# Optimization experiments

Hardware: AMD Instinct MI355X
Metric: run time of the kernel (lower is better)

## Reference

```python
import jax, jax.numpy as jnp
import numpy as np

HEADS = 8
HEAD_DIM = 80
TEXT_LEN = 77


def setup_inputs() -> dict:
    key = jax.random.key(0)
    ks = jax.random.split(key, 10)
    B, S, QD, CD, ID = 16, 4096, 640, 768, 640
    NV = 10
    s = 0.02
    return {
        "x": jax.random.normal(ks[0], (B, S, QD), jnp.float32),
        "enc": jax.random.normal(ks[1], (B, TEXT_LEN + NV, CD), jnp.float32),
        "Wq": jax.random.normal(ks[2], (QD, ID), jnp.float32) * s,
        "Wvq": jax.random.normal(ks[3], (QD, ID), jnp.float32) * s,
        "Wk": jax.random.normal(ks[4], (CD, ID), jnp.float32) * s,
        "Wv": jax.random.normal(ks[5], (CD, ID), jnp.float32) * s,
        "Wvk": jax.random.normal(ks[6], (CD, ID), jnp.float32) * s,
        "Wvv": jax.random.normal(ks[7], (CD, ID), jnp.float32) * s,
        "Wo": jax.random.normal(ks[8], (ID, QD), jnp.float32) * s,
        "bo": jnp.zeros((QD,), jnp.float32),
    }


def reference(x, enc, Wq, Wvq, Wk, Wv, Wvk, Wvv, Wo, bo):
    # x: [B, S, query_dim]; enc: [B, 77 + Nv, cross_dim]
    B, S, _ = x.shape
    H, D = HEADS, HEAD_DIM
    scale = 1.0 / jnp.sqrt(jnp.asarray(D, x.dtype))

    text_feats = enc[:, :TEXT_LEN]      # [B, 77, CD]
    visual_feats = enc[:, TEXT_LEN:]    # [B, Nv, CD]

    tq = (x @ Wq).reshape(B, S, H, D)
    vq = (x @ Wvq).reshape(B, S, H, D)
    tk = (text_feats @ Wk).reshape(B, TEXT_LEN, H, D)
    tv = (text_feats @ Wv).reshape(B, TEXT_LEN, H, D)
    vk = (visual_feats @ Wvk).reshape(B, -1, H, D)
    vv = (visual_feats @ Wvv).reshape(B, -1, H, D)

    # separate score blocks, then concat along key dim
    text_scores = scale * jnp.einsum("bqhd,bkhd->bhqk", tq, tk)
    visual_scores = scale * jnp.einsum("bqhd,bkhd->bhqk", vq, vk)
    scores = jnp.concatenate([text_scores, visual_scores], axis=-1)  # [B,H,S,Kt+Kv]
    probs = jax.nn.softmax(scores, axis=-1)

    value = jnp.concatenate([tv, vv], axis=1)  # [B, Kt+Kv, H, D]
    out = jnp.einsum("bhqk,bkhd->bqhd", probs, value).reshape(B, S, H * D)
    return out @ Wo + bo
```

## Files before the change

### kernel.cpp

```cpp
#include <hip/hip_runtime.h>

typedef __attribute__((ext_vector_type(8))) short short8;
typedef __attribute__((ext_vector_type(4))) float f32x4;
typedef __attribute__((ext_vector_type(4))) int int4v;

typedef const __attribute__((address_space(1))) void* gas_t;
typedef __attribute__((address_space(3))) void* las_t;

__device__ __forceinline__ unsigned short f2bf(float f) {
  unsigned int u = __float_as_uint(f);
  u += 0x7fffu + ((u >> 16) & 1u);
  return (unsigned short)(u >> 16);
}

__global__ void cvt_bf16_kernel(const float* __restrict__ in,
                                unsigned short* __restrict__ out, int n) {
  int i = (blockIdx.x * 256 + threadIdx.x) * 4;
  if (i + 3 < n) {
    float4 v = *(const float4*)(in + i);
    ushort4 r;
    r.x = f2bf(v.x); r.y = f2bf(v.y); r.z = f2bf(v.z); r.w = f2bf(v.w);
    *(ushort4*)(out + i) = r;
  }
}

__global__ void transpose_cvt_kernel(const float* __restrict__ W,
                                     unsigned short* __restrict__ Wt,
                                     int K, int N) {
  __shared__ float t[32][33];
  int tx = threadIdx.x & 31, ty = threadIdx.x >> 5;
  int k0 = blockIdx.x * 32, n0 = blockIdx.y * 32;
  #pragma unroll
  for (int i = 0; i < 32; i += 8)
    t[ty + i][tx] = W[(size_t)(k0 + ty + i) * N + n0 + tx];
  __syncthreads();
  #pragma unroll
  for (int i = 0; i < 32; i += 8)
    Wt[(size_t)(n0 + ty + i) * K + k0 + tx] = f2bf(t[tx][ty + i]);
}

__global__ void vtrans_kernel(const unsigned short* __restrict__ KV,
                              unsigned short* __restrict__ VtG) {
  int idx = blockIdx.x * 256 + threadIdx.x;
  if (idx >= 16 * 8 * 80 * 96) return;
  int k = idx % 96;
  int d = (idx / 96) % 80;
  int h = (idx / (96 * 80)) % 8;
  int b = idx / (96 * 80 * 8);
  unsigned short v = 0;
  if (k < 87) {
    int base = (k < 77) ? 640 : 1920;
    v = KV[(size_t)(b * 87 + k) * 2560 + base + h * 80 + d];
  }
  VtG[idx] = v;
}

template<bool F32OUT>
__global__ __launch_bounds__(256, 2) void gemm_bt_kernel(
    const unsigned short* __restrict__ A,
    const unsigned short* __restrict__ Bt,
    void* __restrict__ Cptr, const float* __restrict__ bias,
    int M, int N, int K, int NT) {
  __shared__ __align__(16) unsigned short smem[2 * 128 * 64];
  unsigned short* As = smem;
  unsigned short* Bs = smem + 128 * 64;

  const int tid  = threadIdx.x;
  const int wave = tid >> 6, lane = tid & 63;
  const int lrow = lane & 15, quad = lane >> 4;

  const int nwg = gridDim.x;
  const int qch = nwg >> 3, rch = nwg & 7;
  const int xcd = blockIdx.x & 7;
  const int wgid = (xcd < rch ? xcd * (qch + 1)
                              : rch * (qch + 1) + (xcd - rch) * qch)
                 + (blockIdx.x >> 3);
  const int row0 = (wgid / NT) * 128, col0 = (wgid % NT) * 128;

  const int wm = (wave >> 1) * 64, wn = (wave & 1) * 64;
  const int srow = lane >> 3;
  const int scol = (lane & 7) * 8;

  f32x4 zero = {0.f, 0.f, 0.f, 0.f};
  f32x4 acc[4][4];
  #pragma unroll
  for (int mi = 0; mi < 4; ++mi)
    #pragma unroll
    for (int ni = 0; ni < 4; ++ni) acc[mi][ni] = zero;

  for (int k0 = 0; k0 < K; k0 += 64) {
    #pragma unroll
    for (int i = 0; i < 4; ++i) {
      int r = (wave * 4 + i) * 8 + srow;
      int ga = row0 + r; if (ga > M - 1) ga = M - 1;
      const unsigned short* gA = A + (size_t)ga * K + k0 + scol;
      __builtin_amdgcn_global_load_lds((gas_t)gA, (las_t)(As + r * 64 + scol), 16, 0, 0);
      const unsigned short* gB = Bt + (size_t)(col0 + r) * K + k0 + scol;
      __builtin_amdgcn_global_load_lds((gas_t)gB, (las_t)(Bs + r * 64 + scol), 16, 0, 0);
    }
    __syncthreads();
    #pragma unroll
    for (int kk = 0; kk < 64; kk += 32) {
      short8 av[4], bv[4];
      #pragma unroll
      for (int mi = 0; mi < 4; ++mi)
        av[mi] = *(const short8*)(As + (wm + mi * 16 + lrow) * 64 + kk + quad * 8);
      #pragma unroll
      for (int ni = 0; ni < 4; ++ni)
        bv[ni] = *(const short8*)(Bs + (wn + ni * 16 + lrow) * 64 + kk + quad * 8);
      #pragma unroll
      for (int mi = 0; mi < 4; ++mi)
        #pragma unroll
        for (int ni = 0; ni < 4; ++ni)
          acc[mi][ni] = __builtin_amdgcn_mfma_f32_16x16x32_bf16(av[mi], bv[ni], acc[mi][ni], 0, 0, 0);
    }
    __syncthreads();
  }

  if (F32OUT) {
    float* C = (float*)Cptr;
    #pragma unroll
    for (int mi = 0; mi < 4; ++mi)
      #pragma unroll
      for (int ni = 0; ni < 4; ++ni) {
        int col = col0 + wn + ni * 16 + lrow;
        float bv = bias[col];
        #pragma unroll
        for (int r = 0; r < 4; ++r) {
          int row = row0 + wm + mi * 16 + quad * 4 + r;
          if (row < M) C[(size_t)row * N + col] = acc[mi][ni][r] + bv;
        }
      }
  } else {
    unsigned short* C = (unsigned short*)Cptr;
    unsigned short* Cw = smem + wave * 4096;
    #pragma unroll
    for (int mi = 0; mi < 4; ++mi)
      #pragma unroll
      for (int ni = 0; ni < 4; ++ni)
        #pragma unroll
        for (int r = 0; r < 4; ++r)
          Cw[(mi * 16 + quad * 4 + r) * 64 + ni * 16 + lrow] = f2bf(acc[mi][ni][r]);
    #pragma unroll
    for (int it = 0; it < 8; ++it) {
      int row = it * 8 + (lane >> 3);
      int c8  = (lane & 7) * 8;
      int grow = row0 + wm + row;
      if (grow < M) {
        int4v v = *(const int4v*)(Cw + row * 64 + c8);
        *(int4v*)(C + (size_t)grow * N + col0 + wn + c8) = v;
      }
    }
  }
}

template<bool F32OUT>
__global__ __launch_bounds__(512, 2) void gemm256_kernel(
    const unsigned short* __restrict__ A,
    const unsigned short* __restrict__ Bt,
    void* __restrict__ Cptr, const float* __restrict__ bias,
    int M, int N, int K, int NT) {
  __shared__ __align__(16) unsigned short smem[4 * 16384];

  const int tid  = threadIdx.x;
  const int wave = tid >> 6, lane = tid & 63;
  const int lrow = lane & 15, quad = lane >> 4;

  const int nwg = gridDim.x;
  const int qch = nwg >> 3, rch = nwg & 7;
  const int xcd = blockIdx.x & 7;
  const int wgid = (xcd < rch ? xcd * (qch + 1)
                              : rch * (qch + 1) + (xcd - rch) * qch)
                 + (blockIdx.x >> 3);
  const int row0 = (wgid / NT) * 256, col0 = (wgid % NT) * 256;

  const int wm = (wave >> 2) * 128;
  const int wn = (wave & 3) * 64;
  const int NKT = K >> 5;

  const unsigned short* gA[2];
  const unsigned short* gB[2];
  #pragma unroll
  for (int j = 0; j < 2; ++j) {
    int P = tid * 16 + j * 8192;
    int lin = P ^ (((P >> 9) & 1) << 5);
    int r = ((P >> 10) << 4) + ((lin >> 6) & 15);
    int c = (lin & 63) >> 1;
    int ga = row0 + r; if (ga > M - 1) ga = M - 1;
    int gb = col0 + r; if (gb > N - 1) gb = N - 1;
    gA[j] = A  + (size_t)ga * K + c;
    gB[j] = Bt + (size_t)gb * K + c;
  }

  const int xorb = ((lrow >> 3) & 1) << 4;
  int offA[8], offB[4];
  #pragma unroll
  for (int mi = 0; mi < 8; ++mi)
    offA[mi] = (((((wm >> 4) + mi) << 9) + (lrow << 5) + (quad << 3))) ^ xorb;
  #pragma unroll
  for (int ni = 0; ni < 4; ++ni)
    offB[ni] = (((((wn >> 4) + ni) << 9) + (lrow << 5) + (quad << 3))) ^ xorb;

  f32x4 zero = {0.f, 0.f, 0.f, 0.f};
  f32x4 acc[8][4];
  #pragma unroll
  for (int mi = 0; mi < 8; ++mi)
    #pragma unroll
    for (int ni = 0; ni < 4; ++ni) acc[mi][ni] = zero;

  #pragma unroll
  for (int t = 0; t < 3; ++t) {
    unsigned short* slot = smem + (t & 3) * 16384;
    #pragma unroll
    for (int j = 0; j < 2; ++j)
      __builtin_amdgcn_global_load_lds((gas_t)(gA[j] + t * 32),
          (las_t)(slot + j * 4096 + tid * 8), 16, 0, 0);
    #pragma unroll
    for (int j = 0; j < 2; ++j)
      __builtin_amdgcn_global_load_lds((gas_t)(gB[j] + t * 32),
          (las_t)(slot + 8192 + j * 4096 + tid * 8), 16, 0, 0);
  }

  for (int t = 0; t < NKT; ++t) {
    if (t + 2 < NKT)      asm volatile("s_waitcnt vmcnt(8)" ::: "memory");
    else if (t + 1 < NKT) asm volatile("s_waitcnt vmcnt(4)" ::: "memory");
    else                  asm volatile("s_waitcnt vmcnt(0)" ::: "memory");
    asm volatile("s_barrier" ::: "memory");

    const unsigned short* As = smem + (t & 3) * 16384;
    const unsigned short* Bs = As + 8192;
    const bool pf = (t + 3 < NKT);
    unsigned short* nslot = smem + ((t + 3) & 3) * 16384;

    short8 av0[4], bv[4];
    #pragma unroll
    for (int mi = 0; mi < 4; ++mi) av0[mi] = *(const short8*)(As + offA[mi]);
    #pragma unroll
    for (int ni = 0; ni < 4; ++ni) bv[ni] = *(const short8*)(Bs + offB[ni]);
    if (pf) {
      #pragma unroll
      for (int j = 0; j < 2; ++j)
        __builtin_amdgcn_global_load_lds((gas_t)(gA[j] + (t + 3) * 32),
            (las_t)(nslot + j * 4096 + tid * 8), 16, 0, 0);
    }
    __builtin_amdgcn_s_setprio(1);
    #pragma unroll
    for (int mi = 0; mi < 4; ++mi)
      #pragma unroll
      for (int ni = 0; ni < 4; ++ni)
        acc[mi][ni] = __builtin_amdgcn_mfma_f32_16x16x32_bf16(av0[mi], bv[ni], acc[mi][ni], 0, 0, 0);
    __builtin_amdgcn_s_setprio(0);

    short8 av1[4];
    #pragma unroll
    for (int mi = 0; mi < 4; ++mi) av1[mi] = *(const short8*)(As + offA[4 + mi]);
    if (pf) {
      #pragma unroll
      for (int j = 0; j < 2; ++j)
        __builtin_amdgcn_global_load_lds((gas_t)(gB[j] + (t + 3) * 32),
            (las_t)(nslot + 8192 + j * 4096 + tid * 8), 16, 0, 0);
    }
    __builtin_amdgcn_s_setprio(1);
    #pragma unroll
    for (int mi = 0; mi < 4; ++mi)
      #pragma unroll
      for (int ni = 0; ni < 4; ++ni)
        acc[4 + mi][ni] = __builtin_amdgcn_mfma_f32_16x16x32_bf16(av1[mi], bv[ni], acc[4 + mi][ni], 0, 0, 0);
    __builtin_amdgcn_s_setprio(0);
  }

  if (F32OUT) {
    float* C = (float*)Cptr;
    #pragma unroll
    for (int mi = 0; mi < 8; ++mi)
      #pragma unroll
      for (int ni = 0; ni < 4; ++ni) {
        int col = col0 + wn + ni * 16 + lrow;
        int colc = col < N ? col : 0;
        float bval = bias[colc];
        #pragma unroll
        for (int r = 0; r < 4; ++r) {
          int row = row0 + wm + mi * 16 + quad * 4 + r;
          if (col < N && row < M)
            C[(size_t)row * N + col] = acc[mi][ni][r] + bval;
        }
      }
  } else {
    asm volatile("s_barrier" ::: "memory");
    unsigned short* C = (unsigned short*)Cptr;
    unsigned short* Cw = smem + wave * 8192;
    #pragma unroll
    for (int mi = 0; mi < 8; ++mi)
      #pragma unroll
      for (int ni = 0; ni < 4; ++ni)
        #pragma unroll
        for (int r = 0; r < 4; ++r)
          Cw[(mi * 16 + quad * 4 + r) * 64 + ni * 16 + lrow] = f2bf(acc[mi][ni][r]);
    #pragma unroll
    for (int it = 0; it < 16; ++it) {
      int row = it * 8 + (lane >> 3);
      int c8  = (lane & 7) * 8;
      int grow = row0 + wm + row;
      if (grow < M) {
        int4v v = *(const int4v*)(Cw + row * 64 + c8);
        *(int4v*)(C + (size_t)grow * N + col0 + wn + c8) = v;
      }
    }
  }
}

__global__ __launch_bounds__(256, 3) void attn_kernel(
    const unsigned short* __restrict__ Q,
    const unsigned short* __restrict__ KV,
    const unsigned short* __restrict__ VtG,
    unsigned short* __restrict__ O) {
  constexpr int KS = 168;
  constexpr int PS = 104;
  __shared__ __align__(16) unsigned short smem[96 * KS + 80 * PS];
  unsigned short* Ke = smem;
  unsigned short* Vt = smem + 96 * KS;
  unsigned short* P  = smem;

  const int tid = threadIdx.x;
  const int wave = tid >> 6, lane = tid & 63;
  const int lrow = lane & 15, quad = lane >> 4;
  const int qt = blockIdx.x, h = blockIdx.y, b = blockIdx.z;
  const size_t qbase = (size_t)(b * 4096 + qt * 64);

  const unsigned short* vg = VtG + (size_t)(b * 8 + h) * 80 * 96;
  for (int idx = tid; idx < 80 * 12; idx += 256) {
    int r = idx / 12, c = idx % 12;
    *(int4v*)(Vt + r * PS + c * 8) = *(const int4v*)(vg + r * 96 + c * 8);
  }
  for (int idx = tid; idx < 96 * 20; idx += 256) {
    int r = idx / 20, c = idx % 20;
    int4v v = {0, 0, 0, 0};
    if (r < 87) {
      if (r < 77 && c < 10)
        v = *(const int4v*)(KV + (size_t)(b * 87 + r) * 2560 + h * 80 + c * 8);
      else if (r >= 77 && c >= 10)
        v = *(const int4v*)(KV + (size_t)(b * 87 + r) * 2560 + 1280 + h * 80 + (c - 10) * 8);
    }
    *(int4v*)(Ke + r * KS + c * 8) = v;
  }

  const unsigned short* Qrow = Q + (qbase + wave * 16 + lrow) * 1280;
  short8 qfrag[5];
  #pragma unroll
  for (int kc = 0; kc < 5; ++kc) {
    int j = kc * 32 + quad * 8;
    int gcol = h * 80 + j + (j >= 80 ? 560 : 0);
    qfrag[kc] = *(const short8*)(Qrow + gcol);
  }
  __syncthreads();

  f32x4 zero = {0.f, 0.f, 0.f, 0.f};
  f32x4 s[6];
  #pragma unroll
  for (int nt = 0; nt < 6; ++nt) s[nt] = zero;
  #pragma unroll
  for (int kc = 0; kc < 5; ++kc) {
    #pragma unroll
    for (int nt = 0; nt < 6; ++nt) {
      short8 bb = *(const short8*)(Ke + (nt * 16 + lrow) * KS + kc * 32 + quad * 8);
      s[nt] = __builtin_amdgcn_mfma_f32_16x16x32_bf16(qfrag[kc], bb, s[nt], 0, 0, 0);
    }
  }

  const float scale = 0.11180339887498949f;
  float mrow[4] = {-1e30f, -1e30f, -1e30f, -1e30f};
  #pragma unroll
  for (int nt = 0; nt < 6; ++nt) {
    bool valid = (nt * 16 + lrow) < 87;
    #pragma unroll
    for (int r = 0; r < 4; ++r) {
      float v = valid ? s[nt][r] * scale : -1e30f;
      s[nt][r] = v;
      mrow[r] = fmaxf(mrow[r], v);
    }
  }
  #pragma unroll
  for (int off = 1; off < 16; off <<= 1)
    #pragma unroll
    for (int r = 0; r < 4; ++r)
      mrow[r] = fmaxf(mrow[r], __shfl_xor(mrow[r], off, 64));
  float lsum[4] = {0.f, 0.f, 0.f, 0.f};
  #pragma unroll
  for (int nt = 0; nt < 6; ++nt)
    #pragma unroll
    for (int r = 0; r < 4; ++r) {
      float p = __expf(s[nt][r] - mrow[r]);
      s[nt][r] = p;
      lsum[r] += p;
    }
  #pragma unroll
  for (int off = 1; off < 16; off <<= 1)
    #pragma unroll
    for (int r = 0; r < 4; ++r)
      lsum[r] += __shfl_xor(lsum[r], off, 64);
  float inv[4];
  #pragma unroll
  for (int r = 0; r < 4; ++r) inv[r] = 1.0f / lsum[r];

  __syncthreads();

  #pragma unroll
  for (int nt = 0; nt < 6; ++nt)
    #pragma unroll
    for (int r = 0; r < 4; ++r)
      P[(wave * 16 + quad * 4 + r) * PS + nt * 16 + lrow] = f2bf(s[nt][r] * inv[r]);

  f32x4 o[5];
  #pragma unroll
  for (int nt = 0; nt < 5; ++nt) o[nt] = zero;
  #pragma unroll
  for (int kc = 0; kc < 3; ++kc) {
    short8 a = *(const short8*)(P + (wave * 16 + lrow) * PS + kc * 32 + quad * 8);
    #pragma unroll
    for (int nt = 0; nt < 5; ++nt) {
      short8 bb = *(const short8*)(Vt + (nt * 16 + lrow) * PS + kc * 32 + quad * 8);
      o[nt] = __builtin_amdgcn_mfma_f32_16x16x32_bf16(a, bb, o[nt], 0, 0, 0);
    }
  }

  unsigned short* Ow = P + wave * 16 * PS;
  #pragma unroll
  for (int nt = 0; nt < 5; ++nt)
    #pragma unroll
    for (int r = 0; r < 4; ++r)
      Ow[(quad * 4 + r) * PS + nt * 16 + lrow] = f2bf(o[nt][r]);
  for (int idx = lane; idx < 160; idx += 64) {
    int r = idx / 10, c = idx % 10;
    *(int4v*)(O + (qbase + wave * 16 + r) * 640 + h * 80 + c * 8) =
        *(const int4v*)(Ow + r * PS + c * 8);
  }
}

extern "C" void kernel_launch(void* const* d_in, const int* in_sizes, int n_in,
                              void* d_out, int out_size, void* d_ws, size_t ws_size,
                              hipStream_t stream) {
  const float* x   = (const float*)d_in[0];
  const float* enc = (const float*)d_in[1];
  const float* Wq  = (const float*)d_in[2];
  const float* Wvq = (const float*)d_in[3];
  const float* Wk  = (const float*)d_in[4];
  const float* Wv  = (const float*)d_in[5];
  const float* Wvk = (const float*)d_in[6];
  const float* Wvv = (const float*)d_in[7];
  const float* Wo  = (const float*)d_in[8];
  const float* bo  = (const float*)d_in[9];
  float* out = (float*)d_out;
  char* ws = (char*)d_ws;

  unsigned short* Qall  = (unsigned short*)(ws);
  unsigned short* xbf   = (unsigned short*)(ws + 167772160ull);
  unsigned short* encbf = (unsigned short*)(ws + 251658240ull);
  unsigned short* KVall = (unsigned short*)(ws + 253796352ull);
  unsigned short* WqcT  = (unsigned short*)(ws + 260923392ull);
  unsigned short* WkvT  = (unsigned short*)(ws + 262561792ull);
  unsigned short* WoT   = (unsigned short*)(ws + 266493952ull);
  unsigned short* VtG   = WkvT;

  cvt_bf16_kernel<<<40960, 256, 0, stream>>>(x, xbf, 41943040);
  cvt_bf16_kernel<<<1044, 256, 0, stream>>>(enc, encbf, 1069056);

  transpose_cvt_kernel<<<dim3(20, 20), 256, 0, stream>>>(Wq,  WqcT,             640, 640);
  transpose_cvt_kernel<<<dim3(20, 20), 256, 0, stream>>>(Wvq, WqcT + 640 * 640, 640, 640);
  transpose_cvt_kernel<<<dim3(24, 20), 256, 0, stream>>>(Wk,  WkvT,              768, 640);
  transpose_cvt_kernel<<<dim3(24, 20), 256, 0, stream>>>(Wv,  WkvT + 640 * 768,  768, 640);
  transpose_cvt_kernel<<<dim3(24, 20), 256, 0, stream>>>(Wvk, WkvT + 1280 * 768, 768, 640);
  transpose_cvt_kernel<<<dim3(24, 20), 256, 0, stream>>>(Wvv, WkvT + 1920 * 768, 768, 640);
  transpose_cvt_kernel<<<dim3(20, 20), 256, 0, stream>>>(Wo,  WoT,              640, 640);

  gemm_bt_kernel<false><<<220, 256, 0, stream>>>(encbf, WkvT, KVall, nullptr, 1392, 2560, 768, 20);
  vtrans_kernel<<<3840, 256, 0, stream>>>(KVall, VtG);
  gemm256_kernel<false><<<1280, 512, 0, stream>>>(xbf, WqcT, Qall, nullptr, 65536, 1280, 640, 5);
  attn_kernel<<<dim3(64, 8, 16), 256, 0, stream>>>(Qall, KVall, VtG, xbf);
  gemm256_kernel<true><<<768, 512, 0, stream>>>(xbf, WoT, out, bo, 65536, 640, 640, 3);
}
```

Measured before the change: 650.0 us.

## Merge prep launches, shrink GEMM LDS to double buffer, widen attention blocks

Merges the two fp32-to-bf16 conversions into one launch and the seven weight transposes into a single 3D-grid launch, cutting launch overhead. The 256x256 GEMM drops from a 4-slot to a 2-slot LDS ring with prefetch issued after a second barrier, and the bf16 epilogue is staged in two halves so the smaller LDS fits. Launch bounds ask for 4 blocks per CU, trading prefetch depth for occupancy. The attention kernel now uses 512 threads covering 128 queries per block, sharing K/V staging across more waves.

```diff
diff --git a/kernel.cpp b/kernel.cpp
--- a/kernel.cpp
+++ b/kernel.cpp
@@ -13,23 +13,49 @@
   return (unsigned short)(u >> 16);
 }
 
-__global__ void cvt_bf16_kernel(const float* __restrict__ in,
-                                unsigned short* __restrict__ out, int n) {
-  int i = (blockIdx.x * 256 + threadIdx.x) * 4;
-  if (i + 3 < n) {
-    float4 v = *(const float4*)(in + i);
+__global__ void cvt2_kernel(const float* __restrict__ x,
+                            unsigned short* __restrict__ xo, int nxb,
+                            const float* __restrict__ enc,
+                            unsigned short* __restrict__ eo, int ne) {
+  if ((int)blockIdx.x < nxb) {
+    int i = (blockIdx.x * 256 + threadIdx.x) * 4;
+    float4 v = *(const float4*)(x + i);
     ushort4 r;
     r.x = f2bf(v.x); r.y = f2bf(v.y); r.z = f2bf(v.z); r.w = f2bf(v.w);
-    *(ushort4*)(out + i) = r;
-  }
-}
-
-__global__ void transpose_cvt_kernel(const float* __restrict__ W,
-                                     unsigned short* __restrict__ Wt,
-                                     int K, int N) {
+    *(ushort4*)(xo + i) = r;
+  } else {
+    int i = ((blockIdx.x - nxb) * 256 + threadIdx.x) * 4;
+    if (i + 3 < ne) {
+      float4 v = *(const float4*)(enc + i);
+      ushort4 r;
+      r.x = f2bf(v.x); r.y = f2bf(v.y); r.z = f2bf(v.z); r.w = f2bf(v.w);
+      *(ushort4*)(eo + i) = r;
+    }
+  }
+}
+
+__global__ void transpose_cvt7_kernel(
+    const float* __restrict__ W0, const float* __restrict__ W1,
+    const float* __restrict__ W2, const float* __restrict__ W3,
+    const float* __restrict__ W4, const float* __restrict__ W5,
+    const float* __restrict__ W6,
+    unsigned short* __restrict__ WqcT, unsigned short* __restrict__ WkvT,
+    unsigned short* __restrict__ WoT) {
+  const float* W; unsigned short* Wt; int K;
+  switch (blockIdx.z) {
+    case 0: W = W0; Wt = WqcT;            K = 640; break;
+    case 1: W = W1; Wt = WqcT + 640*640;  K = 640; break;
+    case 2: W = W2; Wt = WkvT;            K = 768; break;
+    case 3: W = W3; Wt = WkvT + 640*768;  K = 768; break;
+    case 4: W = W4; Wt = WkvT + 1280*768; K = 768; break;
+    case 5: W = W5; Wt = WkvT + 1920*768; K = 768; break;
+    default: W = W6; Wt = WoT;            K = 640; break;
+  }
+  const int N = 640;
+  int k0 = blockIdx.x * 32, n0 = blockIdx.y * 32;
+  if (k0 >= K) return;
   __shared__ float t[32][33];
   int tx = threadIdx.x & 31, ty = threadIdx.x >> 5;
-  int k0 = blockIdx.x * 32, n0 = blockIdx.y * 32;
   #pragma unroll
   for (int i = 0; i < 32; i += 8)
     t[ty + i][tx] = W[(size_t)(k0 + ty + i) * N + n0 + tx];
@@ -155,12 +181,12 @@
 }
 
 template<bool F32OUT>
-__global__ __launch_bounds__(512, 2) void gemm256_kernel(
+__global__ __launch_bounds__(512, 4) void gemm256_kernel(
     const unsigned short* __restrict__ A,
     const unsigned short* __restrict__ Bt,
     void* __restrict__ Cptr, const float* __restrict__ bias,
     int M, int N, int K, int NT) {
-  __shared__ __align__(16) unsigned short smem[4 * 16384];
+  __shared__ __align__(16) unsigned short smem[2 * 16384];
 
   const int tid  = threadIdx.x;
   const int wave = tid >> 6, lane = tid & 63;
@@ -209,8 +235,8 @@
     for (int ni = 0; ni < 4; ++ni) acc[mi][ni] = zero;
 
   #pragma unroll
-  for (int t = 0; t < 3; ++t) {
-    unsigned short* slot = smem + (t & 3) * 16384;
+  for (int t = 0; t < 2; ++t) {
+    unsigned short* slot = smem + t * 16384;
     #pragma unroll
     for (int j = 0; j < 2; ++j)
       __builtin_amdgcn_global_load_lds((gas_t)(gA[j] + t * 32),
@@ -222,27 +248,18 @@
   }
 
   for (int t = 0; t < NKT; ++t) {
-    if (t + 2 < NKT)      asm volatile("s_waitcnt vmcnt(8)" ::: "memory");
-    else if (t + 1 < NKT) asm volatile("s_waitcnt vmcnt(4)" ::: "memory");
-    else                  asm volatile("s_waitcnt vmcnt(0)" ::: "memory");
-    asm volatile("s_barrier" ::: "memory");
-
-    const unsigned short* As = smem + (t & 3) * 16384;
+    if (t + 1 < NKT) asm volatile("s_waitcnt vmcnt(4)" ::: "memory");
+    else             asm volatile("s_waitcnt vmcnt(0)" ::: "memory");
+    __builtin_amdgcn_s_barrier();
+
+    const unsigned short* As = smem + (t & 1) * 16384;
     const unsigned short* Bs = As + 8192;
-    const bool pf = (t + 3 < NKT);
-    unsigned short* nslot = smem + ((t + 3) & 3) * 16384;
 
     short8 av0[4], bv[4];
     #pragma unroll
     for (int mi = 0; mi < 4; ++mi) av0[mi] = *(const short8*)(As + offA[mi]);
     #pragma unroll
     for (int ni = 0; ni < 4; ++ni) bv[ni] = *(const short8*)(Bs + offB[ni]);
-    if (pf) {
-      #pragma unroll
-      for (int j = 0; j < 2; ++j)
-        __builtin_amdgcn_global_load_lds((gas_t)(gA[j] + (t + 3) * 32),
-            (las_t)(nslot + j * 4096 + tid * 8), 16, 0, 0);
-    }
     __builtin_amdgcn_s_setprio(1);
     #pragma unroll
     for (int mi = 0; mi < 4; ++mi)
@@ -254,12 +271,6 @@
     short8 av1[4];
     #pragma unroll
     for (int mi = 0; mi < 4; ++mi) av1[mi] = *(const short8*)(As + offA[4 + mi]);
-    if (pf) {
-      #pragma unroll
-      for (int j = 0; j < 2; ++j)
-        __builtin_amdgcn_global_load_lds((gas_t)(gB[j] + (t + 3) * 32),
-            (las_t)(nslot + 8192 + j * 4096 + tid * 8), 16, 0, 0);
-    }
     __builtin_amdgcn_s_setprio(1);
     #pragma unroll
     for (int mi = 0; mi < 4; ++mi)
@@ -267,6 +278,20 @@
       for (int ni = 0; ni < 4; ++ni)
         acc[4 + mi][ni] = __builtin_amdgcn_mfma_f32_16x16x32_bf16(av1[mi], bv[ni], acc[4 + mi][ni], 0, 0, 0);
     __builtin_amdgcn_s_setprio(0);
+
+    __builtin_amdgcn_s_barrier();
+
+    if (t + 2 < NKT) {
+      unsigned short* nslot = smem + (t & 1) * 16384;
+      #pragma unroll
+      for (int j = 0; j < 2; ++j)
+        __builtin_amdgcn_global_load_lds((gas_t)(gA[j] + (t + 2) * 32),
+            (las_t)(nslot + j * 4096 + tid * 8), 16, 0, 0);
+      #pragma unroll
+      for (int j = 0; j < 2; ++j)
+        __builtin_amdgcn_global_load_lds((gas_t)(gB[j] + (t + 2) * 32),
+            (las_t)(nslot + 8192 + j * 4096 + tid * 8), 16, 0, 0);
+    }
   }
 
   if (F32OUT) {
@@ -286,30 +311,32 @@
         }
       }
   } else {
-    asm volatile("s_barrier" ::: "memory");
     unsigned short* C = (unsigned short*)Cptr;
-    unsigned short* Cw = smem + wave * 8192;
-    #pragma unroll
-    for (int mi = 0; mi < 8; ++mi)
-      #pragma unroll
-      for (int ni = 0; ni < 4; ++ni)
+    unsigned short* Cw = smem + wave * 4096;
+    #pragma unroll
+    for (int p = 0; p < 2; ++p) {
+      #pragma unroll
+      for (int mi = 0; mi < 4; ++mi)
         #pragma unroll
-        for (int r = 0; r < 4; ++r)
-          Cw[(mi * 16 + quad * 4 + r) * 64 + ni * 16 + lrow] = f2bf(acc[mi][ni][r]);
-    #pragma unroll
-    for (int it = 0; it < 16; ++it) {
-      int row = it * 8 + (lane >> 3);
-      int c8  = (lane & 7) * 8;
-      int grow = row0 + wm + row;
-      if (grow < M) {
-        int4v v = *(const int4v*)(Cw + row * 64 + c8);
-        *(int4v*)(C + (size_t)grow * N + col0 + wn + c8) = v;
+        for (int ni = 0; ni < 4; ++ni)
+          #pragma unroll
+          for (int r = 0; r < 4; ++r)
+            Cw[(mi * 16 + quad * 4 + r) * 64 + ni * 16 + lrow] = f2bf(acc[p * 4 + mi][ni][r]);
+      #pragma unroll
+      for (int it = 0; it < 8; ++it) {
+        int row = it * 8 + (lane >> 3);
+        int c8  = (lane & 7) * 8;
+        int grow = row0 + wm + p * 64 + row;
+        if (grow < M) {
+          int4v v = *(const int4v*)(Cw + row * 64 + c8);
+          *(int4v*)(C + (size_t)grow * N + col0 + wn + c8) = v;
+        }
       }
     }
   }
 }
 
-__global__ __launch_bounds__(256, 3) void attn_kernel(
+__global__ __launch_bounds__(512, 4) void attn_kernel(
     const unsigned short* __restrict__ Q,
     const unsigned short* __restrict__ KV,
     const unsigned short* __restrict__ VtG,
@@ -325,14 +352,14 @@
   const int wave = tid >> 6, lane = tid & 63;
   const int lrow = lane & 15, quad = lane >> 4;
   const int qt = blockIdx.x, h = blockIdx.y, b = blockIdx.z;
-  const size_t qbase = (size_t)(b * 4096 + qt * 64);
+  const size_t qbase = (size_t)(b * 4096 + qt * 128);
 
   const unsigned short* vg = VtG + (size_t)(b * 8 + h) * 80 * 96;
-  for (int idx = tid; idx < 80 * 12; idx += 256) {
+  for (int idx = tid; idx < 80 * 12; idx += 512) {
     int r = idx / 12, c = idx % 12;
     *(int4v*)(Vt + r * PS + c * 8) = *(const int4v*)(vg + r * 96 + c * 8);
   }
-  for (int idx = tid; idx < 96 * 20; idx += 256) {
+  for (int idx = tid; idx < 96 * 20; idx += 512) {
     int r = idx / 20, c = idx % 20;
     int4v v = {0, 0, 0, 0};
     if (r < 87) {
@@ -461,20 +488,14 @@
   unsigned short* WoT   = (unsigned short*)(ws + 266493952ull);
   unsigned short* VtG   = WkvT;
 
-  cvt_bf16_kernel<<<40960, 256, 0, stream>>>(x, xbf, 41943040);
-  cvt_bf16_kernel<<<1044, 256, 0, stream>>>(enc, encbf, 1069056);
-
-  transpose_cvt_kernel<<<dim3(20, 20), 256, 0, stream>>>(Wq,  WqcT,             640, 640);
-  transpose_cvt_kernel<<<dim3(20, 20), 256, 0, stream>>>(Wvq, WqcT + 640 * 640, 640, 640);
-  transpose_cvt_kernel<<<dim3(24, 20), 256, 0, stream>>>(Wk,  WkvT,              768, 640);
-  transpose_cvt_kernel<<<dim3(24, 20), 256, 0, stream>>>(Wv,  WkvT + 640 * 768,  768, 640);
-  transpose_cvt_kernel<<<dim3(24, 20), 256, 0, stream>>>(Wvk, WkvT + 1280 * 768, 768, 640);
-  transpose_cvt_kernel<<<dim3(24, 20), 256, 0, stream>>>(Wvv, WkvT + 1920 * 768, 768, 640);
-  transpose_cvt_kernel<<<dim3(20, 20), 256, 0, stream>>>(Wo,  WoT,              640, 640);
+  cvt2_kernel<<<40960 + 1044, 256, 0, stream>>>(x, xbf, 40960, enc, encbf, 1069056);
+
+  transpose_cvt7_kernel<<<dim3(24, 20, 7), 256, 0, stream>>>(
+      Wq, Wvq, Wk, Wv, Wvk, Wvv, Wo, WqcT, WkvT, WoT);
 
   gemm_bt_kernel<false><<<220, 256, 0, stream>>>(encbf, WkvT, KVall, nullptr, 1392, 2560, 768, 20);
   vtrans_kernel<<<3840, 256, 0, stream>>>(KVall, VtG);
   gemm256_kernel<false><<<1280, 512, 0, stream>>>(xbf, WqcT, Qall, nullptr, 65536, 1280, 640, 5);
-  attn_kernel<<<dim3(64, 8, 16), 256, 0, stream>>>(Qall, KVall, VtG, xbf);
+  attn_kernel<<<dim3(32, 8, 16), 512, 0, stream>>>(Qall, KVall, VtG, xbf);
   gemm256_kernel<true><<<768, 512, 0, stream>>>(xbf, WoT, out, bo, 65536, 640, 640, 3);
 }
```

After: 2.161 ms. 232% more time.
